# Optimization experiments

Hardware: AMD Instinct MI355X
Metric: run time of the kernel (lower is better)

The kernel has to match this reference:

```python
import jax, jax.numpy as jnp
import numpy as np

N = 50000       # num_nodes
E = 1_600_000   # num_edges (avg degree 32)
F_IN, HID, F_OUT = 128, 128, 64


def setup_inputs() -> dict:
    key = jax.random.key(0)
    k0, k1, k2, k3 = jax.random.split(key, 4)
    x = jax.random.normal(k0, (1, N, F_IN), dtype=jnp.float32)
    edge_index = jax.random.randint(k1, (2, E), 0, N, dtype=jnp.int32)
    # GCNConv weights (glorot-ish scale) and zero biases
    W1 = jax.random.normal(k2, (F_IN, HID), dtype=jnp.float32) / np.float32(np.sqrt(F_IN))
    b1 = jnp.zeros((HID,), dtype=jnp.float32)
    W2 = jax.random.normal(k3, (HID, F_OUT), dtype=jnp.float32) / np.float32(np.sqrt(HID))
    b2 = jnp.zeros((F_OUT,), dtype=jnp.float32)
    return {"x": x, "edge_index": edge_index, "W1": W1, "b1": b1, "W2": W2, "b2": b2}


def _gcn_layer(h, src, dst, norm, W, b, n):
    # linear transform then symmetric-normalized scatter-add aggregation
    h = h @ W                              # [N, F_out]
    msg = h[src] * norm[:, None]           # [E+N, F_out] gathered messages
    agg = jax.ops.segment_sum(msg, dst, num_segments=n)
    return agg + b


def reference(x, edge_index, W1, b1, W2, b2):
    xn = x[0]                              # [N, F_in] node feature matrix
    n = xn.shape[0]
    src, dst = edge_index[0], edge_index[1]
    # add self-loops (GCNConv default)
    loops = jnp.arange(n, dtype=src.dtype)
    src = jnp.concatenate([src, loops])
    dst = jnp.concatenate([dst, loops])
    # symmetric normalization: deg^-1/2[src] * deg^-1/2[dst] (deg >= 1 w/ self-loops)
    deg = jax.ops.segment_sum(jnp.ones(dst.shape, dtype=xn.dtype), dst, num_segments=n)
    dinv = jax.lax.rsqrt(deg)
    norm = dinv[src] * dinv[dst]
    h = jax.nn.relu(_gcn_layer(xn, src, dst, norm, W1, b1, n))
    out = jax.nn.relu(_gcn_layer(h, src, dst, norm, W2, b2, n))
    return out
```

## Files before the change

kernel.cpp:

```cpp
#include <hip/hip_runtime.h>
#include <hip/hip_fp16.h>


#define TILE 8192
#define BIN_CAP 2560

typedef _Float16 half8 __attribute__((ext_vector_type(8)));
typedef float floatx4 __attribute__((ext_vector_type(4)));

__device__ __forceinline__ void acc8(float* ax, const uint4& u) {
    float2 f;
    f = __half22float2(*(const __half2*)&u.x); ax[0] += f.x; ax[1] += f.y;
    f = __half22float2(*(const __half2*)&u.y); ax[2] += f.x; ax[3] += f.y;
    f = __half22float2(*(const __half2*)&u.z); ax[4] += f.x; ax[5] += f.y;
    f = __half22float2(*(const __half2*)&u.w); ax[6] += f.x; ax[7] += f.y;
}

__global__ __launch_bounds__(512) void bin_kernel(const int* __restrict__ src,
                                                  const int* __restrict__ dst, int E,
                                                  int nbins,
                                                  int* __restrict__ binCnt,
                                                  unsigned* __restrict__ recs) {
    extern __shared__ int lds[];
    int* cnt = lds;
    int* gbase = lds + nbins;
    int tid = threadIdx.x;
    for (int i = tid; i < nbins; i += 512) cnt[i] = 0;
    __syncthreads();

    int t0 = blockIdx.x * TILE;
    int tEnd = min(t0 + TILE, E);

    for (int e = t0 + tid; e < tEnd; e += 512)
        atomicAdd(&cnt[dst[e] >> 6], 1);
    __syncthreads();

    for (int i = tid; i < nbins; i += 512) {
        int c = cnt[i];
        gbase[i] = (c > 0) ? atomicAdd(&binCnt[i], c) : 0;
        cnt[i] = 0;
    }
    __syncthreads();

    for (int e = t0 + tid; e < tEnd; e += 512) {
        int d = dst[e];
        int s = src[e];
        int b = d >> 6;
        int r = atomicAdd(&cnt[b], 1);
        int g = gbase[b] + r;
        if (g < BIN_CAP)
            recs[(size_t)b * BIN_CAP + g] = ((unsigned)(d & 63) << 16) | (unsigned)s;
    }
}

__global__ __launch_bounds__(512) void sort_bins(const unsigned* __restrict__ recs,
                                                 const int* __restrict__ binCnt,
                                                 unsigned short* __restrict__ sortedG,
                                                 int* __restrict__ startG,
                                                 float* __restrict__ dinv, int N) {
    __shared__ unsigned short sorted[BIN_CAP];
    __shared__ int c64[64];
    __shared__ int start[65];
    __shared__ int cursor[64];
    int b = blockIdx.x, tid = threadIdx.x;
    int lane = tid & 63, wave = tid >> 6;

    if (tid < 64) c64[tid] = 0;
    __syncthreads();
    int cnt = min(binCnt[b], BIN_CAP);
    const unsigned* bin = recs + (size_t)b * BIN_CAP;

    for (int i = tid; i < cnt; i += 512)
        atomicAdd(&c64[bin[i] >> 16], 1);
    __syncthreads();

    if (wave == 0) {
        int c = c64[lane];
        int v = c;
        #pragma unroll
        for (int off = 1; off < 64; off <<= 1) {
            int t = __shfl_up(v, off);
            if (lane >= off) v += t;
        }
        start[lane] = v - c;
        cursor[lane] = v - c;
        startG[b * 65 + lane] = v - c;
        if (lane == 63) { start[64] = v; startG[b * 65 + 64] = v; }
        int n = (b << 6) + lane;
        if (n < N) dinv[n] = rsqrtf((float)(c + 1));
    }
    __syncthreads();

    for (int i = tid; i < cnt; i += 512) {
        unsigned r = bin[i];
        int pos = atomicAdd(&cursor[r >> 16], 1);
        sorted[pos] = (unsigned short)(r & 0xFFFFu);
    }
    __syncthreads();
    unsigned short* sg = sortedG + (size_t)b * BIN_CAP;
    for (int i = tid; i < cnt; i += 512) sg[i] = sorted[i];
}

template <int COLS, bool FP32IN>
__global__ __launch_bounds__(256) void gemm_mfma(const void* __restrict__ Xv,
                                                 const float* __restrict__ W,
                                                 const float* __restrict__ dinv,
                                                 __half* __restrict__ Y, int N) {
    constexpr int LDA = 136;
    __shared__ __align__(16) _Float16 aT[64 * LDA];
    __shared__ __align__(16) _Float16 bT[COLS * LDA];

    int tid = threadIdx.x;
    int lane = tid & 63, wave = tid >> 6;
    int row0 = blockIdx.x * 64;

    for (int i = tid * 4; i < 64 * 128; i += 1024) {
        int r = i >> 7, k = i & 127;
        int gr = row0 + r;
        if (FP32IN) {
            float4 v = make_float4(0.f, 0.f, 0.f, 0.f);
            if (gr < N) v = *(const float4*)&((const float*)Xv)[(size_t)gr * 128 + k];
            __half2 p0 = __floats2half2_rn(v.x, v.y);
            __half2 p1 = __floats2half2_rn(v.z, v.w);
            *(uint2*)&aT[r * LDA + k] = make_uint2(*(uint*)&p0, *(uint*)&p1);
        } else {
            ushort4 u = make_ushort4(0, 0, 0, 0);
            if (gr < N) u = *(const ushort4*)&((const __half*)Xv)[(size_t)gr * 128 + k];
            *(ushort4*)&aT[r * LDA + k] = u;
        }
    }
    for (int i = tid; i < 128 * COLS; i += 256) {
        int k = i / COLS, n = i % COLS;
        bT[n * LDA + k] = (_Float16)W[i];
    }
    __syncthreads();

    constexpr int NT = COLS / 16;
    floatx4 acc[NT];
    #pragma unroll
    for (int t = 0; t < NT; t++) acc[t] = (floatx4){0.f, 0.f, 0.f, 0.f};

    int m = lane & 15, q = lane >> 4;
    const _Float16* arow = &aT[(wave * 16 + m) * LDA + q * 8];

    #pragma unroll
    for (int ks = 0; ks < 4; ks++) {
        half8 af = *(const half8*)&arow[ks * 32];
        #pragma unroll
        for (int t = 0; t < NT; t++) {
            half8 bf = *(const half8*)&bT[(t * 16 + m) * LDA + ks * 32 + q * 8];
            acc[t] = __builtin_amdgcn_mfma_f32_16x16x32_f16(af, bf, acc[t], 0, 0, 0);
        }
    }
    __syncthreads();

    float dv[4];
    #pragma unroll
    for (int r = 0; r < 4; r++) {
        int gr = row0 + wave * 16 + q * 4 + r;
        dv[r] = (gr < N) ? dinv[gr] : 0.0f;
    }
    #pragma unroll
    for (int t = 0; t < NT; t++)
        #pragma unroll
        for (int r = 0; r < 4; r++)
            aT[(wave * 16 + q * 4 + r) * LDA + t * 16 + m] = (_Float16)(dv[r] * acc[t][r]);
    __syncthreads();

    for (int i = tid; i < 64 * (COLS / 2); i += 256) {
        int r = i / (COLS / 2), c = i % (COLS / 2);
        int gr = row0 + r;
        if (gr < N)
            ((uint*)Y)[(size_t)gr * (COLS / 2) + c] = *(uint*)&aT[r * LDA + c * 2];
    }
}

__global__ __launch_bounds__(512) void agg_gemm_fused(
        const __half* __restrict__ G,
        const unsigned short* __restrict__ sortedG,
        const int* __restrict__ startG,
        const float* __restrict__ dinv,
        const float* __restrict__ bias,
        const float* __restrict__ W2,
        __half* __restrict__ Y2, int N) {
    constexpr int LDH = 136;
    __shared__ unsigned short buf[BIN_CAP];
    __shared__ int st[65];
    __shared__ __align__(16) _Float16 hT[64 * LDH];
    __shared__ __align__(16) _Float16 bT[64 * LDH];

    int b = blockIdx.x;
    int tid = threadIdx.x, lane = tid & 63, wave = tid >> 6;
    int ql = lane & 15, quad = lane >> 4;

    if (tid < 65) st[tid] = startG[b * 65 + tid];
    __syncthreads();
    int cnt = st[64];
    const unsigned short* sg = sortedG + (size_t)b * BIN_CAP;
    for (int i = tid; i < cnt; i += 512) buf[i] = sg[i];
    for (int i = tid; i < 128 * 64; i += 512) {
        int k = i >> 6, n = i & 63;
        bT[n * LDH + k] = (_Float16)W2[i];
    }
    __syncthreads();

    float bb[8];
    #pragma unroll
    for (int k = 0; k < 4; k++) {
        float2 t = *(const float2*)&bias[ql * 8 + k * 2];
        bb[k * 2] = t.x; bb[k * 2 + 1] = t.y;
    }

    for (int rr = 0; rr < 8; rr++) {
        int row = wave * 8 + rr;
        int n = (b << 6) + row;
        if (n >= N) {
            if (quad == 0) {
                uint4 z = make_uint4(0, 0, 0, 0);
                *(uint4*)&hT[row * LDH + ql * 8] = z;
            }
            continue;
        }
        int jst = st[row], jen = st[row + 1];

        float ax[8] = {};
        int j = jst + quad;
        for (; j + 12 < jen; j += 16) {
            int s0 = buf[j], s1 = buf[j + 4], s2 = buf[j + 8], s3 = buf[j + 12];
            uint4 u0 = *(const uint4*)&G[(size_t)s0 * 128 + ql * 8];
            uint4 u1 = *(const uint4*)&G[(size_t)s1 * 128 + ql * 8];
            uint4 u2 = *(const uint4*)&G[(size_t)s2 * 128 + ql * 8];
            uint4 u3 = *(const uint4*)&G[(size_t)s3 * 128 + ql * 8];
            acc8(ax, u0); acc8(ax, u1); acc8(ax, u2); acc8(ax, u3);
        }
        for (; j < jen; j += 4) {
            int s = buf[j];
            uint4 u = *(const uint4*)&G[(size_t)s * 128 + ql * 8];
            acc8(ax, u);
        }
        #pragma unroll
        for (int k = 0; k < 8; k++) {
            ax[k] += __shfl_xor(ax[k], 16);
            ax[k] += __shfl_xor(ax[k], 32);
        }
        if (quad == 0) {
            uint4 us = *(const uint4*)&G[(size_t)n * 128 + ql * 8];
            acc8(ax, us);
            float di = dinv[n];
            __half2 h[4];
            #pragma unroll
            for (int k = 0; k < 4; k++) {
                float o0 = fmaxf(fmaf(di, ax[k * 2],     bb[k * 2]),     0.0f);
                float o1 = fmaxf(fmaf(di, ax[k * 2 + 1], bb[k * 2 + 1]), 0.0f);
                h[k] = __floats2half2_rn(o0, o1);
            }
            *(uint4*)&hT[row * LDH + ql * 8] = *(uint4*)h;
        }
    }
    __syncthreads();

    int m = lane & 15, q = lane >> 4;
    int mt = wave & 3, nt0 = (wave >> 2) * 2;
    floatx4 acc[2] = {(floatx4){0.f, 0.f, 0.f, 0.f}, (floatx4){0.f, 0.f, 0.f, 0.f}};
    const _Float16* arow = &hT[(mt * 16 + m) * LDH + q * 8];
    #pragma unroll
    for (int ks = 0; ks < 4; ks++) {
        half8 af = *(const half8*)&arow[ks * 32];
        #pragma unroll
        for (int t = 0; t < 2; t++) {
            half8 bf = *(const half8*)&bT[((nt0 + t) * 16 + m) * LDH + ks * 32 + q * 8];
            acc[t] = __builtin_amdgcn_mfma_f32_16x16x32_f16(af, bf, acc[t], 0, 0, 0);
        }
    }
    __syncthreads();

    float dv[4];
    #pragma unroll
    for (int r = 0; r < 4; r++) {
        int gr = (b << 6) + mt * 16 + q * 4 + r;
        dv[r] = (gr < N) ? dinv[gr] : 0.0f;
    }
    #pragma unroll
    for (int t = 0; t < 2; t++)
        #pragma unroll
        for (int r = 0; r < 4; r++)
            hT[(mt * 16 + q * 4 + r) * LDH + (nt0 + t) * 16 + m] = (_Float16)(dv[r] * acc[t][r]);
    __syncthreads();

    for (int i = tid; i < 64 * 32; i += 512) {
        int r = i >> 5, c = i & 31;
        int gr = (b << 6) + r;
        if (gr < N)
            ((uint*)Y2)[(size_t)gr * 32 + c] = *(uint*)&hT[r * LDH + c * 2];
    }
}

__global__ __launch_bounds__(512) void agg_64(const __half* __restrict__ G,
                                              const unsigned short* __restrict__ sortedG,
                                              const int* __restrict__ startG,
                                              const float* __restrict__ dinv,
                                              const float* __restrict__ bias,
                                              float* __restrict__ out, int N) {
    __shared__ unsigned short buf[BIN_CAP];
    __shared__ int st[33];
    int b = blockIdx.x, half_ = blockIdx.y;
    int tid = threadIdx.x, lane = tid & 63, wave = tid >> 6;
    int ol = lane & 7, oct = lane >> 3;
    int r0 = half_ * 32;

    if (tid < 33) st[tid] = startG[b * 65 + r0 + tid];
    __syncthreads();
    int S0 = st[0], S1 = st[32];
    const unsigned short* sg = sortedG + (size_t)b * BIN_CAP;
    for (int i = tid; i < S1 - S0; i += 512) buf[i] = sg[S0 + i];
    __syncthreads();

    float bb[8];
    #pragma unroll
    for (int k = 0; k < 4; k++) {
        float2 t = *(const float2*)&bias[ol * 8 + k * 2];
        bb[k * 2] = t.x; bb[k * 2 + 1] = t.y;
    }

    for (int rr = 0; rr < 4; rr++) {
        int row = wave * 4 + rr;
        int n = (b << 6) + r0 + row;
        if (n >= N) continue;
        int jst = st[row] - S0, jen = st[row + 1] - S0;

        float ax[8] = {};
        int j = jst + oct;
        for (; j + 24 < jen; j += 32) {
            int s0 = buf[j], s1 = buf[j + 8], s2 = buf[j + 16], s3 = buf[j + 24];
            uint4 u0 = *(const uint4*)&G[(size_t)s0 * 64 + ol * 8];
            uint4 u1 = *(const uint4*)&G[(size_t)s1 * 64 + ol * 8];
            uint4 u2 = *(const uint4*)&G[(size_t)s2 * 64 + ol * 8];
            uint4 u3 = *(const uint4*)&G[(size_t)s3 * 64 + ol * 8];
            acc8(ax, u0); acc8(ax, u1); acc8(ax, u2); acc8(ax, u3);
        }
        for (; j < jen; j += 8) {
            int s = buf[j];
            uint4 u = *(const uint4*)&G[(size_t)s * 64 + ol * 8];
            acc8(ax, u);
        }
        #pragma unroll
        for (int k = 0; k < 8; k++) {
            ax[k] += __shfl_xor(ax[k], 8);
            ax[k] += __shfl_xor(ax[k], 16);
            ax[k] += __shfl_xor(ax[k], 32);
        }
        if (oct < 2) {
            uint4 us = *(const uint4*)&G[(size_t)n * 64 + ol * 8];
            acc8(ax, us);
            float di = dinv[n];
            float o[8];
            #pragma unroll
            for (int k = 0; k < 8; k++)
                o[k] = fmaxf(fmaf(di, ax[k], bb[k]), 0.0f);
            if (oct == 0)
                *(float4*)&out[(size_t)n * 64 + ol * 8] = make_float4(o[0], o[1], o[2], o[3]);
            else
                *(float4*)&out[(size_t)n * 64 + ol * 8 + 4] = make_float4(o[4], o[5], o[6], o[7]);
        }
    }
}

extern "C" void kernel_launch(void* const* d_in, const int* in_sizes, int n_in,
                              void* d_out, int out_size, void* d_ws, size_t ws_size,
                              hipStream_t stream) {
    const float* x  = (const float*)d_in[0];
    const int*   ei = (const int*)d_in[1];
    const float* W1 = (const float*)d_in[2];
    const float* b1 = (const float*)d_in[3];
    const float* W2 = (const float*)d_in[4];
    const float* b2 = (const float*)d_in[5];
    float* out = (float*)d_out;

    const int HID  = in_sizes[3];
    const int F_IN = in_sizes[2] / HID;
    const int N    = in_sizes[0] / F_IN;
    const int E    = in_sizes[1] / 2;
    (void)n_in; (void)out_size; (void)ws_size; (void)F_IN;

    const int* src = ei;
    const int* dst = ei + E;

    const int nbins = (N + 63) >> 6;

    char* p = (char*)d_ws;
    auto carve = [&](size_t bytes) { void* q = (void*)p; p += (bytes + 255) & ~(size_t)255; return q; };
    int*            binCnt  = (int*)           carve((size_t)nbins * 4);
    float*          dinv    = (float*)         carve((size_t)N * 4);
    unsigned*       recs    = (unsigned*)      carve((size_t)nbins * BIN_CAP * 4);
    unsigned short* sortedG = (unsigned short*)carve((size_t)nbins * BIN_CAP * 2);
    int*            startG  = (int*)           carve((size_t)nbins * 65 * 4);
    __half*         bufG    = (__half*)        carve((size_t)N * 128 * 2);
    __half*         bufG2   = (__half*)        carve((size_t)N * 64 * 2);

    hipMemsetAsync(binCnt, 0, (size_t)nbins * 4, stream);

    int numTiles = (E + TILE - 1) / TILE;
    size_t binLds = (size_t)nbins * 2 * 4;
    bin_kernel<<<numTiles, 512, binLds, stream>>>(src, dst, E, nbins, binCnt, recs);
    sort_bins<<<nbins, 512, 0, stream>>>(recs, binCnt, sortedG, startG, dinv, N);

    int gemmGrid = (N + 63) / 64;

    gemm_mfma<128, true><<<gemmGrid, 256, 0, stream>>>(x, W1, dinv, bufG, N);

    agg_gemm_fused<<<nbins, 512, 0, stream>>>(bufG, sortedG, startG, dinv, b1, W2, bufG2, N);

    dim3 aggGrid(nbins, 2);
    agg_64<<<aggGrid, 512, 0, stream>>>(bufG2, sortedG, startG, dinv, b2, out, N);
}
```

Before: 227.8 us.

## Merge edge binning with first GEMM and move source dinv scaling into aggregation

Edge binning and the first-layer GEMM now run in one launch, with block ranges split between the two roles, so the GEMM no longer waits for sort_bins to compute dinv. To allow that, the GEMM writes unscaled X·W1, and the first aggregation multiplies each gathered neighbour row by dinv[src] through an extra scalar load per edge. The gather loops in both aggregations are unrolled by two instead of four, which leaves fewer loads in flight per thread but uses fewer registers. The merged kernel uses a static shared buffer that serves both as the bin counters and as the GEMM tiles, and each GEMM block now has 512 threads of which only 4 waves do MFMA.

```diff
diff --git a/kernel.cpp b/kernel.cpp
--- a/kernel.cpp
+++ b/kernel.cpp
@@ -7,6 +7,14 @@
 
 typedef _Float16 half8 __attribute__((ext_vector_type(8)));
 typedef float floatx4 __attribute__((ext_vector_type(4)));
+
+__device__ __forceinline__ void accs8(float* ax, const uint4& u, float d) {
+    float2 f;
+    f = __half22float2(*(const __half2*)&u.x); ax[0] = fmaf(d, f.x, ax[0]); ax[1] = fmaf(d, f.y, ax[1]);
+    f = __half22float2(*(const __half2*)&u.y); ax[2] = fmaf(d, f.x, ax[2]); ax[3] = fmaf(d, f.y, ax[3]);
+    f = __half22float2(*(const __half2*)&u.z); ax[4] = fmaf(d, f.x, ax[4]); ax[5] = fmaf(d, f.y, ax[5]);
+    f = __half22float2(*(const __half2*)&u.w); ax[6] = fmaf(d, f.x, ax[6]); ax[7] = fmaf(d, f.y, ax[7]);
+}
 
 __device__ __forceinline__ void acc8(float* ax, const uint4& u) {
     float2 f;
@@ -16,40 +24,103 @@
     f = __half22float2(*(const __half2*)&u.w); ax[6] += f.x; ax[7] += f.y;
 }
 
-__global__ __launch_bounds__(512) void bin_kernel(const int* __restrict__ src,
-                                                  const int* __restrict__ dst, int E,
-                                                  int nbins,
-                                                  int* __restrict__ binCnt,
-                                                  unsigned* __restrict__ recs) {
-    extern __shared__ int lds[];
-    int* cnt = lds;
-    int* gbase = lds + nbins;
+template <int COLS>
+__global__ __launch_bounds__(512) void bin_gemm(
+        const int* __restrict__ src, const int* __restrict__ dst, int E,
+        int nbins, int numTiles,
+        int* __restrict__ binCnt, unsigned* __restrict__ recs,
+        const float* __restrict__ Xv, const float* __restrict__ W,
+        __half* __restrict__ Y, int N) {
+    constexpr int LDA = 136;
+    __shared__ __align__(16) _Float16 smem[(64 + COLS) * LDA];
     int tid = threadIdx.x;
-    for (int i = tid; i < nbins; i += 512) cnt[i] = 0;
-    __syncthreads();
-
-    int t0 = blockIdx.x * TILE;
-    int tEnd = min(t0 + TILE, E);
-
-    for (int e = t0 + tid; e < tEnd; e += 512)
-        atomicAdd(&cnt[dst[e] >> 6], 1);
-    __syncthreads();
-
-    for (int i = tid; i < nbins; i += 512) {
-        int c = cnt[i];
-        gbase[i] = (c > 0) ? atomicAdd(&binCnt[i], c) : 0;
-        cnt[i] = 0;
-    }
-    __syncthreads();
-
-    for (int e = t0 + tid; e < tEnd; e += 512) {
-        int d = dst[e];
-        int s = src[e];
-        int b = d >> 6;
-        int r = atomicAdd(&cnt[b], 1);
-        int g = gbase[b] + r;
-        if (g < BIN_CAP)
-            recs[(size_t)b * BIN_CAP + g] = ((unsigned)(d & 63) << 16) | (unsigned)s;
+
+    if (blockIdx.x < numTiles) {
+        int* cnt = (int*)smem;
+        int* gbase = cnt + nbins;
+        for (int i = tid; i < nbins; i += 512) cnt[i] = 0;
+        __syncthreads();
+
+        int t0 = blockIdx.x * TILE;
+        int tEnd = min(t0 + TILE, E);
+
+        for (int e = t0 + tid; e < tEnd; e += 512)
+            atomicAdd(&cnt[dst[e] >> 6], 1);
+        __syncthreads();
+
+        for (int i = tid; i < nbins; i += 512) {
+            int c = cnt[i];
+            gbase[i] = (c > 0) ? atomicAdd(&binCnt[i], c) : 0;
+            cnt[i] = 0;
+        }
+        __syncthreads();
+
+        for (int e = t0 + tid; e < tEnd; e += 512) {
+            int d = dst[e];
+            int s = src[e];
+            int b = d >> 6;
+            int r = atomicAdd(&cnt[b], 1);
+            int g = gbase[b] + r;
+            if (g < BIN_CAP)
+                recs[(size_t)b * BIN_CAP + g] = ((unsigned)(d & 63) << 16) | (unsigned)s;
+        }
+        return;
+    }
+
+    int bid = blockIdx.x - numTiles;
+    _Float16* aT = smem;
+    _Float16* bT = smem + 64 * LDA;
+    int lane = tid & 63, wave = tid >> 6;
+    int row0 = bid * 64;
+
+    for (int i = tid * 4; i < 64 * 128; i += 2048) {
+        int r = i >> 7, k = i & 127;
+        int gr = row0 + r;
+        float4 v = make_float4(0.f, 0.f, 0.f, 0.f);
+        if (gr < N) v = *(const float4*)&Xv[(size_t)gr * 128 + k];
+        __half2 p0 = __floats2half2_rn(v.x, v.y);
+        __half2 p1 = __floats2half2_rn(v.z, v.w);
+        *(uint2*)&aT[r * LDA + k] = make_uint2(*(uint*)&p0, *(uint*)&p1);
+    }
+    for (int i = tid; i < 128 * COLS; i += 512) {
+        int k = i / COLS, n = i % COLS;
+        bT[n * LDA + k] = (_Float16)W[i];
+    }
+    __syncthreads();
+
+    constexpr int NT = COLS / 16;
+    int m = lane & 15, q = lane >> 4;
+    floatx4 acc[NT];
+    if (wave < 4) {
+        #pragma unroll
+        for (int t = 0; t < NT; t++) acc[t] = (floatx4){0.f, 0.f, 0.f, 0.f};
+        const _Float16* arow = &aT[(wave * 16 + m) * LDA + q * 8];
+        #pragma unroll
+        for (int ks = 0; ks < 4; ks++) {
+            half8 af = *(const half8*)&arow[ks * 32];
+            #pragma unroll
+            for (int t = 0; t < NT; t++) {
+                half8 bf = *(const half8*)&bT[(t * 16 + m) * LDA + ks * 32 + q * 8];
+                acc[t] = __builtin_amdgcn_mfma_f32_16x16x32_f16(af, bf, acc[t], 0, 0, 0);
+            }
+        }
+    }
+    __syncthreads();
+
+    if (wave < 4) {
+        #pragma unroll
+        for (int t = 0; t < NT; t++)
+            #pragma unroll
+            for (int r = 0; r < 4; r++)
+                aT[(wave * 16 + q * 4 + r) * LDA + t * 16 + m] = (_Float16)acc[t][r];
+    }
+    __syncthreads();
+
+    for (int i = tid; i < 64 * (COLS / 2); i += 512) {
+        int r = i / (COLS / 2), c = i % (COLS / 2);
+        int gr = row0 + r;
+        if (gr < N)
+            ((uint*)Y)[(size_t)gr * (COLS / 2) + c] = *(uint*)&aT[r * LDA + c * 2];
     }
 }
 
@@ -99,80 +170,6 @@
     __syncthreads();
     unsigned short* sg = sortedG + (size_t)b * BIN_CAP;
     for (int i = tid; i < cnt; i += 512) sg[i] = sorted[i];
-}
-
-template <int COLS, bool FP32IN>
-__global__ __launch_bounds__(256) void gemm_mfma(const void* __restrict__ Xv,
-                                                 const float* __restrict__ W,
-                                                 const float* __restrict__ dinv,
-                                                 __half* __restrict__ Y, int N) {
-    constexpr int LDA = 136;
-    __shared__ __align__(16) _Float16 aT[64 * LDA];
-    __shared__ __align__(16) _Float16 bT[COLS * LDA];
-
-    int tid = threadIdx.x;
-    int lane = tid & 63, wave = tid >> 6;
-    int row0 = blockIdx.x * 64;
-
-    for (int i = tid * 4; i < 64 * 128; i += 1024) {
-        int r = i >> 7, k = i & 127;
-        int gr = row0 + r;
-        if (FP32IN) {
-            float4 v = make_float4(0.f, 0.f, 0.f, 0.f);
-            if (gr < N) v = *(const float4*)&((const float*)Xv)[(size_t)gr * 128 + k];
-            __half2 p0 = __floats2half2_rn(v.x, v.y);
-            __half2 p1 = __floats2half2_rn(v.z, v.w);
-            *(uint2*)&aT[r * LDA + k] = make_uint2(*(uint*)&p0, *(uint*)&p1);
-        } else {
-            ushort4 u = make_ushort4(0, 0, 0, 0);
-            if (gr < N) u = *(const ushort4*)&((const __half*)Xv)[(size_t)gr * 128 + k];
-            *(ushort4*)&aT[r * LDA + k] = u;
-        }
-    }
-    for (int i = tid; i < 128 * COLS; i += 256) {
-        int k = i / COLS, n = i % COLS;
-        bT[n * LDA + k] = (_Float16)W[i];
-    }
-    __syncthreads();
-
-    constexpr int NT = COLS / 16;
-    floatx4 acc[NT];
-    #pragma unroll
-    for (int t = 0; t < NT; t++) acc[t] = (floatx4){0.f, 0.f, 0.f, 0.f};
-
-    int m = lane & 15, q = lane >> 4;
-    const _Float16* arow = &aT[(wave * 16 + m) * LDA + q * 8];
-
-    #pragma unroll
-    for (int ks = 0; ks < 4; ks++) {
-        half8 af = *(const half8*)&arow[ks * 32];
-        #pragma unroll
-        for (int t = 0; t < NT; t++) {
-            half8 bf = *(const half8*)&bT[(t * 16 + m) * LDA + ks * 32 + q * 8];
-            acc[t] = __builtin_amdgcn_mfma_f32_16x16x32_f16(af, bf, acc[t], 0, 0, 0);
-        }
-    }
-    __syncthreads();
-
-    float dv[4];
-    #pragma unroll
-    for (int r = 0; r < 4; r++) {
-        int gr = row0 + wave * 16 + q * 4 + r;
-        dv[r] = (gr < N) ? dinv[gr] : 0.0f;
-    }
-    #pragma unroll
-    for (int t = 0; t < NT; t++)
-        #pragma unroll
-        for (int r = 0; r < 4; r++)
-            aT[(wave * 16 + q * 4 + r) * LDA + t * 16 + m] = (_Float16)(dv[r] * acc[t][r]);
-    __syncthreads();
-
-    for (int i = tid; i < 64 * (COLS / 2); i += 256) {
-        int r = i / (COLS / 2), c = i % (COLS / 2);
-        int gr = row0 + r;
-        if (gr < N)
-            ((uint*)Y)[(size_t)gr * (COLS / 2) + c] = *(uint*)&aT[r * LDA + c * 2];
-    }
 }
 
 __global__ __launch_bounds__(512) void agg_gemm_fused(
@@ -225,18 +222,18 @@
 
         float ax[8] = {};
         int j = jst + quad;
-        for (; j + 12 < jen; j += 16) {
-            int s0 = buf[j], s1 = buf[j + 4], s2 = buf[j + 8], s3 = buf[j + 12];
-            uint4 u0 = *(const uint4*)&G[(size_t)s0 * 128 + ql * 8];
-            uint4 u1 = *(const uint4*)&G[(size_t)s1 * 128 + ql * 8];
-            uint4 u2 = *(const uint4*)&G[(size_t)s2 * 128 + ql * 8];
-            uint4 u3 = *(const uint4*)&G[(size_t)s3 * 128 + ql * 8];
-            acc8(ax, u0); acc8(ax, u1); acc8(ax, u2); acc8(ax, u3);
+        for (; j + 4 < jen; j += 8) {
+            int sA = buf[j], sB = buf[j + 4];
+            uint4 uA = *(const uint4*)&G[(size_t)sA * 128 + ql * 8];
+            uint4 uB = *(const uint4*)&G[(size_t)sB * 128 + ql * 8];
+            float dA = dinv[sA], dB = dinv[sB];
+            accs8(ax, uA, dA);
+            accs8(ax, uB, dB);
         }
         for (; j < jen; j += 4) {
             int s = buf[j];
             uint4 u = *(const uint4*)&G[(size_t)s * 128 + ql * 8];
-            acc8(ax, u);
+            accs8(ax, u, dinv[s]);
         }
         #pragma unroll
         for (int k = 0; k < 8; k++) {
@@ -245,8 +242,8 @@
         }
         if (quad == 0) {
             uint4 us = *(const uint4*)&G[(size_t)n * 128 + ql * 8];
-            acc8(ax, us);
             float di = dinv[n];
+            accs8(ax, us, di);
             __half2 h[4];
             #pragma unroll
             for (int k = 0; k < 4; k++) {
@@ -330,13 +327,12 @@
 
         float ax[8] = {};
         int j = jst + oct;
-        for (; j + 24 < jen; j += 32) {
-            int s0 = buf[j], s1 = buf[j + 8], s2 = buf[j + 16], s3 = buf[j + 24];
-            uint4 u0 = *(const uint4*)&G[(size_t)s0 * 64 + ol * 8];
-            uint4 u1 = *(const uint4*)&G[(size_t)s1 * 64 + ol * 8];
-            uint4 u2 = *(const uint4*)&G[(size_t)s2 * 64 + ol * 8];
-            uint4 u3 = *(const uint4*)&G[(size_t)s3 * 64 + ol * 8];
-            acc8(ax, u0); acc8(ax, u1); acc8(ax, u2); acc8(ax, u3);
+        for (; j + 8 < jen; j += 16) {
+            int sA = buf[j], sB = buf[j + 8];
+            uint4 uA = *(const uint4*)&G[(size_t)sA * 64 + ol * 8];
+            uint4 uB = *(const uint4*)&G[(size_t)sB * 64 + ol * 8];
+            acc8(ax, uA);
+            acc8(ax, uB);
         }
         for (; j < jen; j += 8) {
             int s = buf[j];
@@ -400,13 +396,11 @@
     hipMemsetAsync(binCnt, 0, (size_t)nbins * 4, stream);
 
     int numTiles = (E + TILE - 1) / TILE;
-    size_t binLds = (size_t)nbins * 2 * 4;
-    bin_kernel<<<numTiles, 512, binLds, stream>>>(src, dst, E, nbins, binCnt, recs);
+    int gemmGrid = (N + 63) / 64;
+    bin_gemm<128><<<numTiles + gemmGrid, 512, 0, stream>>>(
+        src, dst, E, nbins, numTiles, binCnt, recs, x, W1, bufG, N);
+
     sort_bins<<<nbins, 512, 0, stream>>>(recs, binCnt, sortedG, startG, dinv, N);
-
-    int gemmGrid = (N + 63) / 64;
-
-    gemm_mfma<128, true><<<gemmGrid, 256, 0, stream>>>(x, W1, dinv, bufG, N);
 
     agg_gemm_fused<<<nbins, 512, 0, stream>>>(bufG, sortedG, startG, dinv, b1, W2, bufG2, N);
 
```

After: 205.2 us. -9.9%, faster.
